# Kernel optimization log

Measured on AMD Instinct MI355X. Metric: run time of the kernel, lower is better.

## Reference

```python
import jax, jax.numpy as jnp
import numpy as np

EPS = 1e-6  # AbsMeanFunction eps
LN_EPS = 1e-5


def _absmean_core(W):
    # gamma = mean(|W|) + eps; quantize to {-1, 0, +1}
    gamma = jnp.mean(jnp.abs(W)) + EPS
    Ws = W / gamma
    Wq = jnp.sign(Ws) * jnp.minimum(jnp.round(jnp.abs(Ws)), 1.0)
    return Wq, gamma


@jax.custom_vjp
def absmean(W):
    return _absmean_core(W)[0]


def _absmean_fwd(W):
    Wq, gamma = _absmean_core(W)
    return Wq, gamma


def _absmean_bwd(gamma, g):
    # custom backward from AbsMeanFunction: grad_W = grad_output / gamma
    return (g / gamma,)


absmean.defvjp(_absmean_fwd, _absmean_bwd)


def layernorm(x, w, b, eps=LN_EPS):
    mu = jnp.mean(x, axis=-1, keepdims=True)
    var = jnp.mean((x - mu) ** 2, axis=-1, keepdims=True)
    return (x - mu) * jax.lax.rsqrt(var + eps) * w + b


def setup_inputs() -> dict:
    key = jax.random.key(0)
    k1, k2, k3 = jax.random.split(key, 3)
    d, h = 1024, 4096  # n_embd, mlp_factor * n_embd
    B, T = 8, 2048
    return {
        "x": jax.random.normal(k1, (B, T, d), jnp.float32),
        "W_fc": jax.random.normal(k2, (h, d), jnp.float32),   # BitLinear158 weight (out, in)
        "ln_w": jnp.ones((h,), jnp.float32),
        "ln_b": jnp.zeros((h,), jnp.float32),
        "W_proj": jax.random.normal(k3, (d, h), jnp.float32),  # BitLinear158 weight (out, in)
    }


def reference(x, W_fc, ln_w, ln_b, W_proj):
    # c_fc: ternary-quantized linear, no bias
    h = jnp.einsum('btd,hd->bth', x, absmean(W_fc))
    # exact (erf) GELU matches torch nn.GELU default
    h = jax.nn.gelu(h, approximate=False)
    h = layernorm(h, ln_w, ln_b)
    # c_proj: ternary-quantized linear, no bias; dropout p=0 is identity
    return jnp.einsum('bth,dh->btd', h, absmean(W_proj))
```

## Files before the change

kernel.cpp:

```cpp
#include <hip/hip_runtime.h>
#include <hip/hip_bf16.h>

typedef __attribute__((ext_vector_type(8))) short bf16x8;
typedef __attribute__((ext_vector_type(4))) float f32x4;
typedef unsigned short u16;

#define D_IN  1024
#define D_HID 4096
#define MROWS 16384

__device__ __forceinline__ float b2f(u16 u) {
    union { unsigned int i; float f; } c; c.i = ((unsigned int)u) << 16; return c.f;
}
__device__ __forceinline__ u16 f2b(float f) {
    unsigned int u = __builtin_bit_cast(unsigned int, f);
    return (u16)((u + 0x7FFFu + ((u >> 16) & 1u)) >> 16);
}

__device__ __forceinline__ float gelu_fast(float v) {
    float p = v * fmaf(0.044715f * v, v, 1.0f);
    float e = __builtin_amdgcn_exp2f(-2.302202983f * p);
    return v * __builtin_amdgcn_rcpf(1.0f + e);
}

__global__ void absmean_partial2(const float* __restrict__ W0, const float* __restrict__ W1,
                                 int n4, float* __restrict__ partials) {
    const float* W = blockIdx.y ? W1 : W0;
    float* out = partials + blockIdx.y * 1024;
    __shared__ float sdata[256];
    float s = 0.f;
    const int stride = gridDim.x * blockDim.x;
    for (int i = blockIdx.x * blockDim.x + threadIdx.x; i < n4; i += stride) {
        float4 v = ((const float4*)W)[i];
        s += fabsf(v.x) + fabsf(v.y) + fabsf(v.z) + fabsf(v.w);
    }
    sdata[threadIdx.x] = s;
    __syncthreads();
    for (int off = 128; off > 0; off >>= 1) {
        if (threadIdx.x < off) sdata[threadIdx.x] += sdata[threadIdx.x + off];
        __syncthreads();
    }
    if (threadIdx.x == 0) out[blockIdx.x] = sdata[0];
}

__global__ void absmean_finalize2(const float* __restrict__ partials, float inv_n,
                                  float* __restrict__ gamma) {
    const float* p = partials + blockIdx.x * 1024;
    __shared__ float sdata[256];
    float s = 0.f;
    for (int i = threadIdx.x; i < 1024; i += 256) s += p[i];
    sdata[threadIdx.x] = s;
    __syncthreads();
    for (int off = 128; off > 0; off >>= 1) {
        if (threadIdx.x < off) sdata[threadIdx.x] += sdata[threadIdx.x + off];
        __syncthreads();
    }
    if (threadIdx.x == 0) gamma[blockIdx.x] = sdata[0] * inv_n + 1e-6f;
}

__global__ void quant_ternary2(const float* __restrict__ W0, const float* __restrict__ W1,
                               const float* __restrict__ gamma,
                               u16* __restrict__ Q0, u16* __restrict__ Q1, int n4) {
    const float* W = blockIdx.y ? W1 : W0;
    u16* Wq = blockIdx.y ? Q1 : Q0;
    const float thr = 0.5f * gamma[blockIdx.y];
    const int stride = gridDim.x * blockDim.x;
    for (int i = blockIdx.x * blockDim.x + threadIdx.x; i < n4; i += stride) {
        float4 v = ((const float4*)W)[i];
        ushort4 q;
        q.x = v.x > thr ? 0x3F80u : (v.x < -thr ? 0xBF80u : 0u);
        q.y = v.y > thr ? 0x3F80u : (v.y < -thr ? 0xBF80u : 0u);
        q.z = v.z > thr ? 0x3F80u : (v.z < -thr ? 0xBF80u : 0u);
        q.w = v.w > thr ? 0x3F80u : (v.w < -thr ? 0xBF80u : 0u);
        ((ushort4*)Wq)[i] = q;
    }
}

__global__ void cast_to_bf16(const float* __restrict__ x, u16* __restrict__ xb, int n8) {
    const int stride = gridDim.x * blockDim.x;
    for (int i = blockIdx.x * blockDim.x + threadIdx.x; i < n8; i += stride) {
        float4 a = ((const float4*)x)[2 * i];
        float4 c = ((const float4*)x)[2 * i + 1];
        bf16x8 o;
        o[0] = (short)f2b(a.x); o[1] = (short)f2b(a.y); o[2] = (short)f2b(a.z); o[3] = (short)f2b(a.w);
        o[4] = (short)f2b(c.x); o[5] = (short)f2b(c.y); o[6] = (short)f2b(c.z); o[7] = (short)f2b(c.w);
        ((bf16x8*)xb)[i] = o;
    }
}

template <int EPI>
__global__ __launch_bounds__(512, 2)
void gemm256(const u16* __restrict__ A, const u16* __restrict__ B,
             void* __restrict__ Cout, int M, int N, int K, int nbx)
{
    (void)M;
    __shared__ u16 lds[65536];
    char* const ldsc = (char*)lds;
    const int tid = threadIdx.x;
    const int w = tid >> 6, lane = tid & 63;

    const int nwg = (int)gridDim.x;
    const int qq = nwg >> 3;
    const int bid = (int)blockIdx.x;
    const int swz = (bid & 7) * qq + (bid >> 3);
    const int bx = swz % nbx, by = swz / nbx;
    const size_t m0 = (size_t)by * 256, n0 = (size_t)bx * 256;

    const int wm = (w >> 2) * 128;
    const int wn = (w & 3) * 64;

    const int d0 = tid * 16;
    const int rrow = (d0 >> 6) & 15;
    const int sr0 = ((d0 >> 11) & 3) * 16 + rrow;
    const int cbx = (d0 & 63) ^ (((rrow >> 3) & 1) << 5);
    const int gc  = ((d0 >> 10) & 1) * 32 + (cbx >> 1);

    const int laneoffsw = (((lane & 15) * 64) + ((lane >> 4) * 16)) ^ (((lane >> 3) & 1) << 5);
    const int aoff = ((wm >> 7) << 14) + laneoffsw;
    const int boff = 65536 + ((wn >> 7) << 14) + (((wn >> 4) & 7) << 11) + laneoffsw;

    f32x4 acc[8][4];
#pragma unroll
    for (int i = 0; i < 8; ++i)
#pragma unroll
        for (int j = 0; j < 4; ++j) acc[i][j] = (f32x4){0.f, 0.f, 0.f, 0.f};

    bf16x8 a[4][2], b[4][2];

#define STAGE_A(KT, BUFB, HH) do {                                                              \
    const u16* _s = A + (size_t)(m0 + (HH) * 128 + sr0) * K + (size_t)(KT) * 64 + gc;           \
    __builtin_amdgcn_global_load_lds((const __attribute__((address_space(1))) void*)_s,         \
        (__attribute__((address_space(3))) void*)(ldsc + (BUFB) * 32768 + (HH) * 16384 + w * 1024), 16, 0, 0); \
    __builtin_amdgcn_global_load_lds((const __attribute__((address_space(1))) void*)(_s + (size_t)64 * K), \
        (__attribute__((address_space(3))) void*)(ldsc + (BUFB) * 32768 + (HH) * 16384 + w * 1024 + 8192), 16, 0, 0); \
} while (0)

#define STAGE_B(KT, BUFB, HH) do {                                                              \
    const u16* _s = B + (size_t)(n0 + (HH) * 128 + sr0) * K + (size_t)(KT) * 64 + gc;           \
    __builtin_amdgcn_global_load_lds((const __attribute__((address_space(1))) void*)_s,         \
        (__attribute__((address_space(3))) void*)(ldsc + 65536 + (BUFB) * 32768 + (HH) * 16384 + w * 1024), 16, 0, 0); \
    __builtin_amdgcn_global_load_lds((const __attribute__((address_space(1))) void*)(_s + (size_t)64 * K), \
        (__attribute__((address_space(3))) void*)(ldsc + 65536 + (BUFB) * 32768 + (HH) * 16384 + w * 1024 + 8192), 16, 0, 0); \
} while (0)

#define RD_A(BUFB, S, KS) (*(const bf16x8*)(ldsc + (BUFB) * 32768 + aoff + ((S) << 11) + ((KS) << 10)))
#define RD_B(BUFB, S, KS) (*(const bf16x8*)(ldsc + (BUFB) * 32768 + boff + ((S) << 11) + ((KS) << 10)))

#define MM(MB, NB) do {                                                                         \
    _Pragma("unroll") for (int ii = 0; ii < 4; ++ii)                                            \
    _Pragma("unroll") for (int jj = 0; jj < 2; ++jj)                                            \
    _Pragma("unroll") for (int kk = 0; kk < 2; ++kk)                                            \
        acc[(MB) + ii][(NB) + jj] = __builtin_amdgcn_mfma_f32_16x16x32_bf16(                    \
            a[ii][kk], b[(NB) + jj][kk], acc[(MB) + ii][(NB) + jj], 0, 0, 0);                   \
} while (0)

#define BARR()  asm volatile("s_barrier" ::: "memory")
#define LGKM0() asm volatile("s_waitcnt lgkmcnt(0)" ::: "memory")

#define ITER(F) do {                                                                            \
                                                \
    _Pragma("unroll") for (int s = 0; s < 4; ++s) { a[s][0] = RD_A(0, s, 0); a[s][1] = RD_A(0, s, 1); } \
    _Pragma("unroll") for (int s = 0; s < 2; ++s) { b[s][0] = RD_B(0, s, 0); b[s][1] = RD_B(0, s, 1); } \
    STAGE_A(t + 1, 1, 0);                                                                       \
    asm volatile("s_waitcnt lgkmcnt(8)" ::: "memory");                                          \
    BARR(); LGKM0();                                                                            \
    __builtin_amdgcn_s_setprio(1); MM(0, 0); __builtin_amdgcn_s_setprio(0); BARR();             \
                                                        \
    _Pragma("unroll") for (int s = 2; s < 4; ++s) { b[s][0] = RD_B(0, s, 0); b[s][1] = RD_B(0, s, 1); } \
    STAGE_A(t + 1, 1, 1);                                                                       \
    BARR(); LGKM0();                                                                            \
    __builtin_amdgcn_s_setprio(1); MM(0, 2); __builtin_amdgcn_s_setprio(0); BARR();             \
                                                        \
    _Pragma("unroll") for (int s = 0; s < 4; ++s) { a[s][0] = RD_A(0, 4 + s, 0); a[s][1] = RD_A(0, 4 + s, 1); } \
    if (F) STAGE_B(t + 2, 0, 0);                                                                \
    BARR(); LGKM0();                                                                            \
    __builtin_amdgcn_s_setprio(1); MM(4, 0); __builtin_amdgcn_s_setprio(0); BARR();             \
                            \
    if (F) { STAGE_B(t + 2, 0, 1); asm volatile("s_waitcnt vmcnt(4)" ::: "memory"); }           \
    else   { asm volatile("s_waitcnt vmcnt(0)" ::: "memory"); }                                 \
    BARR();                                                                                     \
    __builtin_amdgcn_s_setprio(1); MM(4, 2); __builtin_amdgcn_s_setprio(0); BARR();             \
                                                \
    _Pragma("unroll") for (int s = 0; s < 4; ++s) { a[s][0] = RD_A(1, s, 0); a[s][1] = RD_A(1, s, 1); } \
    _Pragma("unroll") for (int s = 0; s < 2; ++s) { b[s][0] = RD_B(1, s, 0); b[s][1] = RD_B(1, s, 1); } \
    if (F) STAGE_A(t + 2, 0, 0);                                                                \
    asm volatile("s_waitcnt lgkmcnt(8)" ::: "memory");                                          \
    BARR(); LGKM0();                                                                            \
    __builtin_amdgcn_s_setprio(1); MM(0, 0); __builtin_amdgcn_s_setprio(0); BARR();             \
                                                        \
    _Pragma("unroll") for (int s = 2; s < 4; ++s) { b[s][0] = RD_B(1, s, 0); b[s][1] = RD_B(1, s, 1); } \
    if (F) STAGE_A(t + 2, 0, 1);                                                                \
    BARR(); LGKM0();                                                                            \
    __builtin_amdgcn_s_setprio(1); MM(0, 2); __builtin_amdgcn_s_setprio(0); BARR();             \
                                                        \
    _Pragma("unroll") for (int s = 0; s < 4; ++s) { a[s][0] = RD_A(1, 4 + s, 0); a[s][1] = RD_A(1, 4 + s, 1); } \
    if (F) STAGE_B(t + 3, 1, 0);                                                                \
    BARR(); LGKM0();                                                                            \
    __builtin_amdgcn_s_setprio(1); MM(4, 0); __builtin_amdgcn_s_setprio(0); BARR();             \
                            \
    if (F) { STAGE_B(t + 3, 1, 1); asm volatile("s_waitcnt vmcnt(4)" ::: "memory"); }           \
    BARR();                                                                                     \
    __builtin_amdgcn_s_setprio(1); MM(4, 2); __builtin_amdgcn_s_setprio(0); BARR();             \
} while (0)

    const int nkt = K >> 6;
    const int niter = nkt >> 1;

    STAGE_A(0, 0, 0);
    STAGE_A(0, 0, 1);
    STAGE_B(0, 0, 0);
    STAGE_B(0, 0, 1);
    STAGE_B(1, 1, 0);
    STAGE_B(1, 1, 1);
    asm volatile("s_waitcnt vmcnt(4)" ::: "memory");
    BARR();

    for (int it = 0; it + 1 < niter; ++it) { const int t = 2 * it; ITER(1); }
    { const int t = 2 * (niter - 1); ITER(0); }

    const int fr = (lane >> 4) * 4;
    const int fc = lane & 15;
    if constexpr (EPI == 0) {
        u16* C = (u16*)Cout;
#pragma unroll
        for (int mf = 0; mf < 8; ++mf)
#pragma unroll
            for (int nf = 0; nf < 4; ++nf)
#pragma unroll
                for (int r = 0; r < 4; ++r) {
                    size_t row = m0 + wm + mf * 16 + fr + r;
                    size_t col = n0 + wn + nf * 16 + fc;
                    C[row * (size_t)N + col] = f2b(gelu_fast(acc[mf][nf][r]));
                }
    } else {
        float* C = (float*)Cout;
#pragma unroll
        for (int mf = 0; mf < 8; ++mf)
#pragma unroll
            for (int nf = 0; nf < 4; ++nf)
#pragma unroll
                for (int r = 0; r < 4; ++r) {
                    size_t row = m0 + wm + mf * 16 + fr + r;
                    size_t col = n0 + wn + nf * 16 + fc;
                    C[row * (size_t)N + col] = acc[mf][nf][r];
                }
    }
#undef STAGE_A
#undef STAGE_B
#undef RD_A
#undef RD_B
#undef MM
#undef BARR
#undef LGKM0
#undef ITER
}

__global__ __launch_bounds__(256)
void ln_rows(u16* __restrict__ h, const float* __restrict__ w, const float* __restrict__ b) {
    const int H = 4096;
    u16* row = h + (size_t)blockIdx.x * H;
    const int t = threadIdx.x;
    bf16x8 v0 = ((bf16x8*)row)[2 * t];
    bf16x8 v1 = ((bf16x8*)row)[2 * t + 1];
    float vals[16];
#pragma unroll
    for (int e = 0; e < 8; ++e) { vals[e] = b2f((u16)v0[e]); vals[8 + e] = b2f((u16)v1[e]); }
    float s = 0.f, ss = 0.f;
#pragma unroll
    for (int e = 0; e < 16; ++e) { s += vals[e]; ss += vals[e] * vals[e]; }
#pragma unroll
    for (int off = 32; off > 0; off >>= 1) {
        s  += __shfl_down(s, off);
        ss += __shfl_down(ss, off);
    }
    __shared__ float sh_s[4], sh_ss[4];
    const int wave = t >> 6, lane = t & 63;
    if (lane == 0) { sh_s[wave] = s; sh_ss[wave] = ss; }
    __syncthreads();
    s  = sh_s[0] + sh_s[1] + sh_s[2] + sh_s[3];
    ss = sh_ss[0] + sh_ss[1] + sh_ss[2] + sh_ss[3];
    const float mu = s * (1.f / 4096.f);
    const float var = ss * (1.f / 4096.f) - mu * mu;
    const float rstd = rsqrtf(var + 1e-5f);
    const int c0 = t * 16;
    bf16x8 o0, o1;
#pragma unroll
    for (int e = 0; e < 8; ++e) {
        o0[e] = (short)f2b((vals[e]     - mu) * rstd * w[c0 + e]     + b[c0 + e]);
        o1[e] = (short)f2b((vals[8 + e] - mu) * rstd * w[c0 + 8 + e] + b[c0 + 8 + e]);
    }
    ((bf16x8*)row)[2 * t]     = o0;
    ((bf16x8*)row)[2 * t + 1] = o1;
}

extern "C" void kernel_launch(void* const* d_in, const int* in_sizes, int n_in,
                              void* d_out, int out_size, void* d_ws, size_t ws_size,
                              hipStream_t stream)
{
    const float* x   = (const float*)d_in[0];
    const float* Wfc = (const float*)d_in[1];
    const float* lnw = (const float*)d_in[2];
    const float* lnb = (const float*)d_in[3];
    const float* Wpj = (const float*)d_in[4];
    float* out = (float*)d_out;
    char* ws = (char*)d_ws;

    u16* Wq_fc = (u16*)ws;
    u16* Wq_pj = (u16*)(ws + (size_t)(8u  << 20));
    u16* xb    = (u16*)(ws + (size_t)(16u << 20));
    u16* hbuf  = (u16*)(ws + (size_t)(48u << 20));
    float* tail = (float*)(ws + (size_t)(176u << 20));
    float* parts = tail;
    float* gam   = tail + 2048;

    const int nW  = D_HID * D_IN;
    const int nW4 = nW / 4;

    absmean_partial2<<<dim3(1024, 2), 256, 0, stream>>>(Wfc, Wpj, nW4, parts);
    absmean_finalize2<<<2, 256, 0, stream>>>(parts, 1.f / (float)nW, gam);
    quant_ternary2<<<dim3(1024, 2), 256, 0, stream>>>(Wfc, Wpj, gam, Wq_fc, Wq_pj, nW4);

    const int nX8 = MROWS * D_IN / 8;
    cast_to_bf16<<<2048, 256, 0, stream>>>(x, xb, nX8);

    {
        const int nbx = D_HID / 256;
        const int nby = MROWS / 256;
        gemm256<0><<<dim3(nbx * nby), dim3(512), 0, stream>>>(xb, Wq_fc, hbuf, MROWS, D_HID, D_IN, nbx);
    }

    ln_rows<<<MROWS, 256, 0, stream>>>(hbuf, lnw, lnb);

    {
        const int nbx = D_IN / 256;
        const int nby = MROWS / 256;
        gemm256<1><<<dim3(nbx * nby), dim3(512), 0, stream>>>(hbuf, Wq_pj, out, MROWS, D_IN, D_HID, nbx);
    }
}
```

Baseline: 426.2 us.

## Fold LayerNorm into projection GEMM via row stats and weight-folded affine

Removes the separate LayerNorm pass over the hidden activations. The first GEMM epilogue now emits per-row partial sum and sum-of-squares of the GELU output, and a small kernel turns them into per-row scale and shift. ln_w is folded into the ternary projection weights, and ln_b plus the mean term become per-column constants added in the second GEMM epilogue. The weight-prep and x-cast kernels are also merged into fewer launches. The cost is extra reduction work and an LDS barrier in the GEMM1 epilogue, and the projection weights are no longer pure ternary, so precision differs slightly.

```diff
diff --git a/kernel.cpp b/kernel.cpp
--- a/kernel.cpp
+++ b/kernel.cpp
@@ -23,10 +23,24 @@
     return v * __builtin_amdgcn_rcpf(1.0f + e);
 }
 
-__global__ void absmean_partial2(const float* __restrict__ W0, const float* __restrict__ W1,
-                                 int n4, float* __restrict__ partials) {
-    const float* W = blockIdx.y ? W1 : W0;
-    float* out = partials + blockIdx.y * 1024;
+__global__ void prep1(const float* __restrict__ x, const float* __restrict__ W0,
+                      const float* __restrict__ W1, u16* __restrict__ xb,
+                      float* __restrict__ partials, int n4, int n8) {
+    const int y = blockIdx.y;
+    if (y == 2) {
+        const int stride = gridDim.x * blockDim.x;
+        for (int i = blockIdx.x * blockDim.x + threadIdx.x; i < n8; i += stride) {
+            float4 a = ((const float4*)x)[2 * i];
+            float4 c = ((const float4*)x)[2 * i + 1];
+            bf16x8 o;
+            o[0] = (short)f2b(a.x); o[1] = (short)f2b(a.y); o[2] = (short)f2b(a.z); o[3] = (short)f2b(a.w);
+            o[4] = (short)f2b(c.x); o[5] = (short)f2b(c.y); o[6] = (short)f2b(c.z); o[7] = (short)f2b(c.w);
+            ((bf16x8*)xb)[i] = o;
+        }
+        return;
+    }
+    const float* W = y ? W1 : W0;
+    float* out = partials + y * 1024;
     __shared__ float sdata[256];
     float s = 0.f;
     const int stride = gridDim.x * blockDim.x;
@@ -58,40 +72,81 @@
     if (threadIdx.x == 0) gamma[blockIdx.x] = sdata[0] * inv_n + 1e-6f;
 }
 
-__global__ void quant_ternary2(const float* __restrict__ W0, const float* __restrict__ W1,
-                               const float* __restrict__ gamma,
-                               u16* __restrict__ Q0, u16* __restrict__ Q1, int n4) {
-    const float* W = blockIdx.y ? W1 : W0;
-    u16* Wq = blockIdx.y ? Q1 : Q0;
-    const float thr = 0.5f * gamma[blockIdx.y];
+__global__ void prep2(const float* __restrict__ W0, const float* __restrict__ W1,
+                      const float* __restrict__ lnw, const float* __restrict__ lnb,
+                      const float* __restrict__ gamma,
+                      u16* __restrict__ Q0, u16* __restrict__ Q1,
+                      float* __restrict__ c1, float* __restrict__ c0, int n4) {
+    const int y = blockIdx.y;
+    if (y == 2) {
+        const float thr = 0.5f * gamma[1];
+        const float* row = W1 + (size_t)blockIdx.x * D_HID;
+        float s1 = 0.f, s0 = 0.f;
+        for (int h = threadIdx.x; h < D_HID; h += 256) {
+            float v = row[h];
+            float t = v > thr ? 1.f : (v < -thr ? -1.f : 0.f);
+            s1 += lnw[h] * t;
+            s0 += lnb[h] * t;
+        }
+#pragma unroll
+        for (int off = 32; off > 0; off >>= 1) {
+            s1 += __shfl_down(s1, off);
+            s0 += __shfl_down(s0, off);
+        }
+        __shared__ float sh1[4], sh0[4];
+        const int wave = threadIdx.x >> 6, lane = threadIdx.x & 63;
+        if (lane == 0) { sh1[wave] = s1; sh0[wave] = s0; }
+        __syncthreads();
+        if (threadIdx.x == 0) {
+            c1[blockIdx.x] = sh1[0] + sh1[1] + sh1[2] + sh1[3];
+            c0[blockIdx.x] = sh0[0] + sh0[1] + sh0[2] + sh0[3];
+        }
+        return;
+    }
+    const float* W = y ? W1 : W0;
+    u16* Wq = y ? Q1 : Q0;
+    const float thr = 0.5f * gamma[y];
     const int stride = gridDim.x * blockDim.x;
     for (int i = blockIdx.x * blockDim.x + threadIdx.x; i < n4; i += stride) {
         float4 v = ((const float4*)W)[i];
         ushort4 q;
-        q.x = v.x > thr ? 0x3F80u : (v.x < -thr ? 0xBF80u : 0u);
-        q.y = v.y > thr ? 0x3F80u : (v.y < -thr ? 0xBF80u : 0u);
-        q.z = v.z > thr ? 0x3F80u : (v.z < -thr ? 0xBF80u : 0u);
-        q.w = v.w > thr ? 0x3F80u : (v.w < -thr ? 0xBF80u : 0u);
+        if (y == 0) {
+            q.x = v.x > thr ? 0x3F80u : (v.x < -thr ? 0xBF80u : 0u);
+            q.y = v.y > thr ? 0x3F80u : (v.y < -thr ? 0xBF80u : 0u);
+            q.z = v.z > thr ? 0x3F80u : (v.z < -thr ? 0xBF80u : 0u);
+            q.w = v.w > thr ? 0x3F80u : (v.w < -thr ? 0xBF80u : 0u);
+        } else {
+            const int h = (i * 4) & (D_HID - 1);
+            float w0 = lnw[h], w1 = lnw[h + 1], w2 = lnw[h + 2], w3 = lnw[h + 3];
+            q.x = v.x > thr ? f2b(w0) : (v.x < -thr ? f2b(-w0) : 0u);
+            q.y = v.y > thr ? f2b(w1) : (v.y < -thr ? f2b(-w1) : 0u);
+            q.z = v.z > thr ? f2b(w2) : (v.z < -thr ? f2b(-w2) : 0u);
+            q.w = v.w > thr ? f2b(w3) : (v.w < -thr ? f2b(-w3) : 0u);
+        }
         ((ushort4*)Wq)[i] = q;
     }
 }
 
-__global__ void cast_to_bf16(const float* __restrict__ x, u16* __restrict__ xb, int n8) {
-    const int stride = gridDim.x * blockDim.x;
-    for (int i = blockIdx.x * blockDim.x + threadIdx.x; i < n8; i += stride) {
-        float4 a = ((const float4*)x)[2 * i];
-        float4 c = ((const float4*)x)[2 * i + 1];
-        bf16x8 o;
-        o[0] = (short)f2b(a.x); o[1] = (short)f2b(a.y); o[2] = (short)f2b(a.z); o[3] = (short)f2b(a.w);
-        o[4] = (short)f2b(c.x); o[5] = (short)f2b(c.y); o[6] = (short)f2b(c.z); o[7] = (short)f2b(c.w);
-        ((bf16x8*)xb)[i] = o;
-    }
+__global__ void finalize_stats(const float* __restrict__ pS, const float* __restrict__ pSS,
+                               float* __restrict__ stA, float* __restrict__ stB) {
+    const int r = blockIdx.x * 256 + threadIdx.x;
+    float s = 0.f, ss = 0.f;
+#pragma unroll
+    for (int b = 0; b < 16; ++b) { s += pS[b * MROWS + r]; ss += pSS[b * MROWS + r]; }
+    const float mu = s * (1.f / (float)D_HID);
+    const float var = ss * (1.f / (float)D_HID) - mu * mu;
+    const float A = rsqrtf(var + 1e-5f);
+    stA[r] = A;
+    stB[r] = -mu * A;
 }
 
 template <int EPI>
 __global__ __launch_bounds__(512, 2)
 void gemm256(const u16* __restrict__ A, const u16* __restrict__ B,
-             void* __restrict__ Cout, int M, int N, int K, int nbx)
+             void* __restrict__ Cout, int M, int N, int K, int nbx,
+             float* __restrict__ pS, float* __restrict__ pSS,
+             const float* __restrict__ stA, const float* __restrict__ stB,
+             const float* __restrict__ c1t, const float* __restrict__ c0t)
 {
     (void)M;
     __shared__ u16 lds[65536];
@@ -158,46 +213,38 @@
 #define LGKM0() asm volatile("s_waitcnt lgkmcnt(0)" ::: "memory")
 
 #define ITER(F) do {                                                                            \
-                                                \
     _Pragma("unroll") for (int s = 0; s < 4; ++s) { a[s][0] = RD_A(0, s, 0); a[s][1] = RD_A(0, s, 1); } \
     _Pragma("unroll") for (int s = 0; s < 2; ++s) { b[s][0] = RD_B(0, s, 0); b[s][1] = RD_B(0, s, 1); } \
     STAGE_A(t + 1, 1, 0);                                                                       \
     asm volatile("s_waitcnt lgkmcnt(8)" ::: "memory");                                          \
     BARR(); LGKM0();                                                                            \
     __builtin_amdgcn_s_setprio(1); MM(0, 0); __builtin_amdgcn_s_setprio(0); BARR();             \
-                                                        \
     _Pragma("unroll") for (int s = 2; s < 4; ++s) { b[s][0] = RD_B(0, s, 0); b[s][1] = RD_B(0, s, 1); } \
     STAGE_A(t + 1, 1, 1);                                                                       \
     BARR(); LGKM0();                                                                            \
     __builtin_amdgcn_s_setprio(1); MM(0, 2); __builtin_amdgcn_s_setprio(0); BARR();             \
-                                                        \
     _Pragma("unroll") for (int s = 0; s < 4; ++s) { a[s][0] = RD_A(0, 4 + s, 0); a[s][1] = RD_A(0, 4 + s, 1); } \
     if (F) STAGE_B(t + 2, 0, 0);                                                                \
     BARR(); LGKM0();                                                                            \
     __builtin_amdgcn_s_setprio(1); MM(4, 0); __builtin_amdgcn_s_setprio(0); BARR();             \
-                            \
     if (F) { STAGE_B(t + 2, 0, 1); asm volatile("s_waitcnt vmcnt(4)" ::: "memory"); }           \
     else   { asm volatile("s_waitcnt vmcnt(0)" ::: "memory"); }                                 \
     BARR();                                                                                     \
     __builtin_amdgcn_s_setprio(1); MM(4, 2); __builtin_amdgcn_s_setprio(0); BARR();             \
-                                                \
     _Pragma("unroll") for (int s = 0; s < 4; ++s) { a[s][0] = RD_A(1, s, 0); a[s][1] = RD_A(1, s, 1); } \
     _Pragma("unroll") for (int s = 0; s < 2; ++s) { b[s][0] = RD_B(1, s, 0); b[s][1] = RD_B(1, s, 1); } \
     if (F) STAGE_A(t + 2, 0, 0);                                                                \
     asm volatile("s_waitcnt lgkmcnt(8)" ::: "memory");                                          \
     BARR(); LGKM0();                                                                            \
     __builtin_amdgcn_s_setprio(1); MM(0, 0); __builtin_amdgcn_s_setprio(0); BARR();             \
-                                                        \
     _Pragma("unroll") for (int s = 2; s < 4; ++s) { b[s][0] = RD_B(1, s, 0); b[s][1] = RD_B(1, s, 1); } \
     if (F) STAGE_A(t + 2, 0, 1);                                                                \
     BARR(); LGKM0();                                                                            \
     __builtin_amdgcn_s_setprio(1); MM(0, 2); __builtin_amdgcn_s_setprio(0); BARR();             \
-                                                        \
     _Pragma("unroll") for (int s = 0; s < 4; ++s) { a[s][0] = RD_A(1, 4 + s, 0); a[s][1] = RD_A(1, 4 + s, 1); } \
     if (F) STAGE_B(t + 3, 1, 0);                                                                \
     BARR(); LGKM0();                                                                            \
     __builtin_amdgcn_s_setprio(1); MM(4, 0); __builtin_amdgcn_s_setprio(0); BARR();             \
-                            \
     if (F) { STAGE_B(t + 3, 1, 1); asm volatile("s_waitcnt vmcnt(4)" ::: "memory"); }           \
     BARR();                                                                                     \
     __builtin_amdgcn_s_setprio(1); MM(4, 2); __builtin_amdgcn_s_setprio(0); BARR();             \
@@ -221,29 +268,59 @@
     const int fr = (lane >> 4) * 4;
     const int fc = lane & 15;
     if constexpr (EPI == 0) {
+        float* redS  = (float*)ldsc;
+        float* redSS = (float*)(ldsc + 4096);
+        const int wnq = w & 3;
         u16* C = (u16*)Cout;
 #pragma unroll
         for (int mf = 0; mf < 8; ++mf)
 #pragma unroll
-            for (int nf = 0; nf < 4; ++nf)
-#pragma unroll
-                for (int r = 0; r < 4; ++r) {
-                    size_t row = m0 + wm + mf * 16 + fr + r;
-                    size_t col = n0 + wn + nf * 16 + fc;
-                    C[row * (size_t)N + col] = f2b(gelu_fast(acc[mf][nf][r]));
+            for (int r = 0; r < 4; ++r) {
+                const int lrow = wm + mf * 16 + fr + r;
+                const size_t row = m0 + lrow;
+                float s = 0.f, ss = 0.f;
+#pragma unroll
+                for (int nf = 0; nf < 4; ++nf) {
+                    float g = gelu_fast(acc[mf][nf][r]);
+                    C[row * (size_t)N + (n0 + wn + nf * 16 + fc)] = f2b(g);
+                    s += g;
+                    ss = fmaf(g, g, ss);
                 }
+#pragma unroll
+                for (int mask = 1; mask < 16; mask <<= 1) {
+                    s  += __shfl_xor(s, mask);
+                    ss += __shfl_xor(ss, mask);
+                }
+                if (fc == 0) { redS[wnq * 256 + lrow] = s; redSS[wnq * 256 + lrow] = ss; }
+            }
+        __syncthreads();
+        if (tid < 256) {
+            float s  = redS[tid]  + redS[256 + tid]  + redS[512 + tid]  + redS[768 + tid];
+            float ss = redSS[tid] + redSS[256 + tid] + redSS[512 + tid] + redSS[768 + tid];
+            pS[(size_t)bx * MROWS + m0 + tid]  = s;
+            pSS[(size_t)bx * MROWS + m0 + tid] = ss;
+        }
     } else {
         float* C = (float*)Cout;
+        float c1v[4], c0v[4];
+#pragma unroll
+        for (int nf = 0; nf < 4; ++nf) {
+            const size_t col = n0 + wn + nf * 16 + fc;
+            c1v[nf] = c1t[col];
+            c0v[nf] = c0t[col];
+        }
 #pragma unroll
         for (int mf = 0; mf < 8; ++mf)
 #pragma unroll
-            for (int nf = 0; nf < 4; ++nf)
-#pragma unroll
-                for (int r = 0; r < 4; ++r) {
-                    size_t row = m0 + wm + mf * 16 + fr + r;
-                    size_t col = n0 + wn + nf * 16 + fc;
-                    C[row * (size_t)N + col] = acc[mf][nf][r];
+            for (int r = 0; r < 4; ++r) {
+                const size_t row = m0 + wm + mf * 16 + fr + r;
+                const float Av = stA[row], Bv = stB[row];
+#pragma unroll
+                for (int nf = 0; nf < 4; ++nf) {
+                    const size_t col = n0 + wn + nf * 16 + fc;
+                    C[row * (size_t)N + col] = fmaf(Av, acc[mf][nf][r], fmaf(Bv, c1v[nf], c0v[nf]));
                 }
+            }
     }
 #undef STAGE_A
 #undef STAGE_B
@@ -253,44 +330,6 @@
 #undef BARR
 #undef LGKM0
 #undef ITER
-}
-
-__global__ __launch_bounds__(256)
-void ln_rows(u16* __restrict__ h, const float* __restrict__ w, const float* __restrict__ b) {
-    const int H = 4096;
-    u16* row = h + (size_t)blockIdx.x * H;
-    const int t = threadIdx.x;
-    bf16x8 v0 = ((bf16x8*)row)[2 * t];
-    bf16x8 v1 = ((bf16x8*)row)[2 * t + 1];
-    float vals[16];
-#pragma unroll
-    for (int e = 0; e < 8; ++e) { vals[e] = b2f((u16)v0[e]); vals[8 + e] = b2f((u16)v1[e]); }
-    float s = 0.f, ss = 0.f;
-#pragma unroll
-    for (int e = 0; e < 16; ++e) { s += vals[e]; ss += vals[e] * vals[e]; }
-#pragma unroll
-    for (int off = 32; off > 0; off >>= 1) {
-        s  += __shfl_down(s, off);
-        ss += __shfl_down(ss, off);
-    }
-    __shared__ float sh_s[4], sh_ss[4];
-    const int wave = t >> 6, lane = t & 63;
-    if (lane == 0) { sh_s[wave] = s; sh_ss[wave] = ss; }
-    __syncthreads();
-    s  = sh_s[0] + sh_s[1] + sh_s[2] + sh_s[3];
-    ss = sh_ss[0] + sh_ss[1] + sh_ss[2] + sh_ss[3];
-    const float mu = s * (1.f / 4096.f);
-    const float var = ss * (1.f / 4096.f) - mu * mu;
-    const float rstd = rsqrtf(var + 1e-5f);
-    const int c0 = t * 16;
-    bf16x8 o0, o1;
-#pragma unroll
-    for (int e = 0; e < 8; ++e) {
-        o0[e] = (short)f2b((vals[e]     - mu) * rstd * w[c0 + e]     + b[c0 + e]);
-        o1[e] = (short)f2b((vals[8 + e] - mu) * rstd * w[c0 + 8 + e] + b[c0 + 8 + e]);
-    }
-    ((bf16x8*)row)[2 * t]     = o0;
-    ((bf16x8*)row)[2 * t + 1] = o1;
 }
 
 extern "C" void kernel_launch(void* const* d_in, const int* in_sizes, int n_in,
@@ -309,31 +348,37 @@
     u16* Wq_pj = (u16*)(ws + (size_t)(8u  << 20));
     u16* xb    = (u16*)(ws + (size_t)(16u << 20));
     u16* hbuf  = (u16*)(ws + (size_t)(48u << 20));
-    float* tail = (float*)(ws + (size_t)(176u << 20));
-    float* parts = tail;
-    float* gam   = tail + 2048;
+    char* tail = ws + (size_t)(176u << 20);
+    float* parts = (float*)tail;
+    float* gam   = (float*)(tail + 8192);
+    float* stA   = (float*)(tail + 16384);
+    float* stB   = (float*)(tail + 16384 + 65536);
+    float* c1t   = (float*)(tail + 16384 + 131072);
+    float* c0t   = (float*)(tail + 16384 + 131072 + 4096);
+    float* pS    = (float*)(ws + (size_t)(177u << 20));
+    float* pSS   = (float*)(ws + (size_t)(178u << 20));
 
     const int nW  = D_HID * D_IN;
     const int nW4 = nW / 4;
-
-    absmean_partial2<<<dim3(1024, 2), 256, 0, stream>>>(Wfc, Wpj, nW4, parts);
+    const int nX8 = MROWS * D_IN / 8;
+
+    prep1<<<dim3(1024, 3), 256, 0, stream>>>(x, Wfc, Wpj, xb, parts, nW4, nX8);
     absmean_finalize2<<<2, 256, 0, stream>>>(parts, 1.f / (float)nW, gam);
-    quant_ternary2<<<dim3(1024, 2), 256, 0, stream>>>(Wfc, Wpj, gam, Wq_fc, Wq_pj, nW4);
-
-    const int nX8 = MROWS * D_IN / 8;
-    cast_to_bf16<<<2048, 256, 0, stream>>>(x, xb, nX8);
+    prep2<<<dim3(1024, 3), 256, 0, stream>>>(Wfc, Wpj, lnw, lnb, gam, Wq_fc, Wq_pj, c1t, c0t, nW4);
 
     {
         const int nbx = D_HID / 256;
         const int nby = MROWS / 256;
-        gemm256<0><<<dim3(nbx * nby), dim3(512), 0, stream>>>(xb, Wq_fc, hbuf, MROWS, D_HID, D_IN, nbx);
-    }
-
-    ln_rows<<<MROWS, 256, 0, stream>>>(hbuf, lnw, lnb);
+        gemm256<0><<<dim3(nbx * nby), dim3(512), 0, stream>>>(
+            xb, Wq_fc, hbuf, MROWS, D_HID, D_IN, nbx, pS, pSS, nullptr, nullptr, nullptr, nullptr);
+    }
+
+    finalize_stats<<<64, 256, 0, stream>>>(pS, pSS, stA, stB);
 
     {
         const int nbx = D_IN / 256;
         const int nby = MROWS / 256;
-        gemm256<1><<<dim3(nbx * nby), dim3(512), 0, stream>>>(hbuf, Wq_pj, out, MROWS, D_IN, D_HID, nbx);
-    }
-}
+        gemm256<1><<<dim3(nbx * nby), dim3(512), 0, stream>>>(
+            hbuf, Wq_pj, out, MROWS, D_IN, D_HID, nbx, nullptr, nullptr, stA, stB, c1t, c0t);
+    }
+}
```

New measurement: 411.1 us. 3.5% less time.
